# Performance work log

Measured on AMD Instinct MI355X. Metric: run time of the kernel, lower is better.

The kernel has to match this reference:

```python
import jax, jax.numpy as jnp
import numpy as np

ITERS = 10  # resonator iterations (iterations=10 in init_kwargs)

def _bipolar(key, shape):
    return jnp.where(jax.random.normal(key, shape) >= 0, 1.0, -1.0).astype(jnp.float32)

def setup_inputs() -> dict:
    key = jax.random.key(0)
    k1, k2, k3 = jax.random.split(key, 3)
    b, f, v, d = 64, 4, 256, 16384
    input_ = _bipolar(k1, (b, d))
    init_estimates = _bipolar(k2, (b, f, d))
    codebooks = _bipolar(k3, (f, v, d))
    return {"input": input_, "init_estimates": init_estimates, "codebooks": codebooks}

def _sign(x):
    # multiset quantize: bipolar sign (ties -> +1), matching MAP-VSA quantization
    return jnp.where(x >= 0, 1.0, -1.0).astype(x.dtype)

def reference(input, init_estimates, codebooks):
    """CONCURRENT resonator, SOFTWARE mode, activation=NONE, stoch=NONE.
    input: (b, d) bipolar; init_estimates: (b, f, d); codebooks: (f, v, d).
    For bipolar vectors: bind = elementwise *, inverse = identity, so
    multibind of all-but-factor-j equals (product over all f) * estimate_j
    (since e*e = 1). This replaces the roll+stack+multibind with one fused pass.
    """
    def step(est, _):
        total = jnp.prod(est, axis=-2, keepdims=True)        # (b, 1, d)
        inv_others = total * est                             # (b, f, d) product of other factors
        new_est = input[:, None, :] * inv_others             # unbind: (b, f, d)
        sim = jnp.einsum('bfd,fvd->bfv', new_est, codebooks) # dot_similarity
        # multiset(codebook, similarity, quantize=True): sign of similarity-weighted sum
        est_new = _sign(jnp.einsum('bfv,fvd->bfd', sim, codebooks))
        return est_new, None
    est, _ = jax.lax.scan(step, init_estimates, None, length=ITERS)
    # cleanup: argmax of |similarity| per factor (argmax_abs=True)
    sim = jnp.einsum('bfd,fvd->bfv', est, codebooks)
    outcome = jnp.argmax(jnp.abs(sim), axis=-1)              # (b, f) codeword indices
    return est, outcome
```

## Files before the change

### kernel.cpp

```cpp
#include <hip/hip_runtime.h>
#include <stdint.h>

typedef unsigned long long ull;
typedef unsigned short ushort_t;
typedef __attribute__((ext_vector_type(8))) short bf16x8;
typedef __attribute__((ext_vector_type(4))) float f32x4;


__global__ void pack_bits(const float* __restrict__ src, ull* __restrict__ dst, int nwords) {
    int gw   = (int)((blockIdx.x * blockDim.x + threadIdx.x) >> 6);
    int lane = threadIdx.x & 63;
    if (gw >= nwords) return;
    float x = src[(size_t)gw * 64 + lane];
    ull m = __ballot(x < 0.0f);
    if (lane == 0) dst[gw] = m;
}

__global__ void pack_cbw(const float* __restrict__ cb, ull* __restrict__ cbw) {
    int gw   = (int)((blockIdx.x * blockDim.x + threadIdx.x) >> 6);
    int lane = threadIdx.x & 63;
    int f = gw >> 16, rem = gw & 65535, w = rem >> 8, v = rem & 255;
    float x = cb[(size_t)(f * 256 + v) * 16384 + (size_t)w * 64 + lane];
    ull m = __ballot(x < 0.0f);
    if (lane == 0) cbw[(size_t)(f * 256 + w) * 256 + v] = m;
}

__global__ void pack_cbT(const ull* __restrict__ cbw, ull* __restrict__ cbT) {
    int gw   = (int)((blockIdx.x * blockDim.x + threadIdx.x) >> 6);
    int lane = threadIdx.x & 63;
    int f = gw >> 16, rem = gw & 65535, j = rem >> 14, d = rem & 16383;
    ull w = cbw[(size_t)(f * 256 + (d >> 6)) * 256 + j * 64 + lane];
    ull m = __ballot((w >> (d & 63)) & 1ull);
    if (lane == 0) cbT[(size_t)(f * 4 + j) * 16384 + d] = m;
}

__global__ void make_offc(const ull* __restrict__ cbT, int* __restrict__ offc) {
    int i = blockIdx.x * 256 + threadIdx.x;
    int f = i >> 14, d = i & 16383;
    int npop = 0;
    #pragma unroll
    for (int j = 0; j < 4; ++j) npop += __popcll(cbT[((size_t)f * 4 + j) * 16384 + d]);
    offc[i] = 8192 * (256 - 2 * npop);
}

__device__ __forceinline__ ushort_t f2bf(int x) {
    return (ushort_t)(__float_as_uint((float)x) >> 16);
}

__global__ __launch_bounds__(512) void simA_kernel(
        const ull* __restrict__ in_bits, const ull* __restrict__ est_in,
        const ull* __restrict__ cbw, ushort_t* __restrict__ simAB) {
    int b = blockIdx.x >> 2, f = blockIdx.x & 3;
    __shared__ ull s_ne[256];
    __shared__ short s_hp[2][256];
    int t = threadIdx.x;
    if (t < 256) {
        ull e0 = est_in[(size_t)(b * 4 + 0) * 256 + t];
        ull e1 = est_in[(size_t)(b * 4 + 1) * 256 + t];
        ull e2 = est_in[(size_t)(b * 4 + 2) * 256 + t];
        ull e3 = est_in[(size_t)(b * 4 + 3) * 256 + t];
        ull u  = in_bits[(size_t)b * 256 + t] ^ e0 ^ e1 ^ e2 ^ e3;
        ull ef = (f == 0) ? e0 : ((f == 1) ? e1 : ((f == 2) ? e2 : e3));
        s_ne[t] = u ^ ef;
    }
    __syncthreads();
    int v = t & 255, half = t >> 8;
    const ull* cw = cbw + (size_t)f * 65536 + (size_t)(half * 128) * 256 + v;
    int acc = 0;
    #pragma unroll 8
    for (int w = 0; w < 128; ++w)
        acc += __popcll(s_ne[half * 128 + w] ^ cw[(size_t)w * 256]);
    s_hp[half][v] = (short)acc;
    __syncthreads();
    if (t < 256) {
        int q = 16384 - (s_hp[0][t] + s_hp[1][t]);
        size_t base = ((size_t)(f * 64 + b)) * 512 + t;
        simAB[base]       = f2bf(q >> 8);
        simAB[base + 256] = f2bf(q & 255);
    }
}

__global__ __launch_bounds__(256) void gemm_kernel(
        const ull* __restrict__ cbT, const ushort_t* __restrict__ simAB,
        const int* __restrict__ offc, ull* __restrict__ est_out) {
    int f = blockIdx.x >> 6, dblk = blockIdx.x & 63;
    __shared__ int4 sB[8192];
    __shared__ unsigned char s_sign[64][256];
    __shared__ int s_off[256];
    int t = threadIdx.x;
    int lane = t & 63, wave = t >> 6;

    if (t < 256) s_off[t] = offc[f * 16384 + dblk * 256 + t];

    #pragma unroll 4
    for (int it = 0; it < 32; ++it) {
        int flat = it * 256 + t;
        int kc = flat >> 10, nt = (flat >> 6) & 15, l = flat & 63;
        int v0 = kc * 32 + ((l >> 4) << 3);
        int d  = dblk * 256 + nt * 16 + (l & 15);
        ull w = cbT[((size_t)f * 4 + (v0 >> 6)) * 16384 + d];
        unsigned bits = (unsigned)(w >> (v0 & 63)) & 0xFFu;
        int4 val;
        val.x = 0x3F803F80 | ((bits & 1u) << 15)        | ((bits & 2u) << 30);
        val.y = 0x3F803F80 | (((bits >> 2) & 1u) << 15) | (((bits >> 2) & 2u) << 30);
        val.z = 0x3F803F80 | (((bits >> 4) & 1u) << 15) | (((bits >> 4) & 2u) << 30);
        val.w = 0x3F803F80 | (((bits >> 6) & 1u) << 15) | (((bits >> 6) & 2u) << 30);
        sB[flat] = val;
    }

    bf16x8 Ahi[8], Alo[8];
    int m0 = wave * 16;
    const ushort_t* abase = simAB + ((size_t)(f * 64 + m0 + (lane & 15))) * 512 + ((lane >> 4) << 3);
    #pragma unroll
    for (int kc = 0; kc < 8; ++kc) {
        Ahi[kc] = *(const bf16x8*)(abase + kc * 32);
        Alo[kc] = *(const bf16x8*)(abase + 256 + kc * 32);
    }
    __syncthreads();

    for (int nt = 0; nt < 16; ++nt) {
        f32x4 acch = {0.f, 0.f, 0.f, 0.f}, accl = {0.f, 0.f, 0.f, 0.f};
        #pragma unroll
        for (int kc = 0; kc < 8; ++kc) {
            bf16x8 B = *(const bf16x8*)&sB[(kc * 16 + nt) * 64 + lane];
            acch = __builtin_amdgcn_mfma_f32_16x16x32_bf16(Ahi[kc], B, acch, 0, 0, 0);
            accl = __builtin_amdgcn_mfma_f32_16x16x32_bf16(Alo[kc], B, accl, 0, 0, 0);
        }
        int dl = nt * 16 + (lane & 15);
        float offf = (float)s_off[dl];
        #pragma unroll
        for (int r = 0; r < 4; ++r) {
            float S = 256.0f * acch[r] + accl[r];
            s_sign[m0 + ((lane >> 4) << 2) + r][dl] = (S < offf) ? 1 : 0;
        }
    }
    __syncthreads();

    if (t < 256) {
        int b = t >> 2, w = t & 3;
        ull m = 0;
        #pragma unroll
        for (int j2 = 0; j2 < 64; ++j2)
            m |= ((ull)s_sign[b][w * 64 + j2]) << j2;
        est_out[((size_t)(b * 4 + f)) * 256 + dblk * 4 + w] = m;
    }
}

__global__ __launch_bounds__(1024) void final_kernel(
        const ull* __restrict__ est, const ull* __restrict__ cbw, float* __restrict__ out) {
    int b = blockIdx.x >> 2, f = blockIdx.x & 3;
    __shared__ ull s_e[256];
    __shared__ int s_part[4][256];
    __shared__ int s_sim[256];
    int t = threadIdx.x;
    if (t < 256) s_e[t] = est[(size_t)(b * 4 + f) * 256 + t];
    __syncthreads();
    {
        int q = t >> 8, v = t & 255;
        const ull* cw = cbw + (size_t)f * 65536 + (size_t)(q * 64) * 256 + v;
        int acc = 0;
        #pragma unroll 8
        for (int w = 0; w < 64; ++w)
            acc += __popcll(s_e[q * 64 + w] ^ cw[(size_t)w * 256]);
        s_part[q][v] = acc;
    }
    __syncthreads();
    if (t < 256) {
        int h = s_part[0][t] + s_part[1][t] + s_part[2][t] + s_part[3][t];
        s_sim[t] = 16384 - 2 * h;
    }
    __syncthreads();
    int wv = t >> 6, lane = t & 63;
    if (wv == 0) {
        int best_a = -1, best_v = 0;
        #pragma unroll
        for (int c = 0; c < 4; ++c) {
            int v = c * 64 + lane;
            int sv = s_sim[v];
            int a = sv < 0 ? -sv : sv;
            if (a > best_a) { best_a = a; best_v = v; }
        }
        #pragma unroll
        for (int off = 1; off < 64; off <<= 1) {
            int oa = __shfl_xor(best_a, off);
            int ov = __shfl_xor(best_v, off);
            if (oa > best_a || (oa == best_a && ov < best_v)) { best_a = oa; best_v = ov; }
        }
        if (lane == 0) out[4194304 + b * 4 + f] = (float)best_v;
    }
    #pragma unroll
    for (int i = 0; i < 16; ++i) {
        int d = i * 1024 + t;
        ull w = s_e[d >> 6];
        out[((size_t)(b * 4 + f) << 14) + d] = ((w >> (d & 63)) & 1ull) ? -1.0f : 1.0f;
    }
}

extern "C" void kernel_launch(void* const* d_in, const int* in_sizes, int n_in,
                              void* d_out, int out_size, void* d_ws, size_t ws_size,
                              hipStream_t stream) {
    const float* input    = (const float*)d_in[0];
    const float* init_est = (const float*)d_in[1];
    const float* cb       = (const float*)d_in[2];
    float* out = (float*)d_out;
    char* ws = (char*)d_ws;

    ull* in_bits    = (ull*)(ws + 0);
    ull* est0       = (ull*)(ws + 131072);
    ull* est1       = (ull*)(ws + 655360);
    ull* cbw        = (ull*)(ws + 1179648);
    ull* cbT        = (ull*)(ws + 3276800);
    ushort_t* simAB = (ushort_t*)(ws + 5373952);
    int* offc       = (int*)(ws + 5636096);

    pack_bits<<<4096, 256, 0, stream>>>(input, in_bits, 16384);
    pack_bits<<<16384, 256, 0, stream>>>(init_est, est0, 65536);
    pack_cbw<<<65536, 256, 0, stream>>>(cb, cbw);
    pack_cbT<<<65536, 256, 0, stream>>>(cbw, cbT);
    make_offc<<<256, 256, 0, stream>>>(cbT, offc);

    ull* bufs[2] = { est0, est1 };
    for (int i = 0; i < 10; ++i) {
        simA_kernel<<<256, 512, 0, stream>>>(in_bits, bufs[i & 1], cbw, simAB);
        gemm_kernel<<<256, 256, 0, stream>>>(cbT, simAB, offc, bufs[(i & 1) ^ 1]);
    }
    final_kernel<<<256, 1024, 0, stream>>>(est0, cbw, out);
}
```

Before: 375.2 us.

## Merge pack kernels, widen blocks, ballot-pack gemm signs, fold offset into gemm

Merges the two input-packing launches into one and makes pack_cbw iterate in the read order of the float codebook so loads coalesce. The separate make_offc kernel is removed and its offsets are computed inside each gemm block. simA and gemm now run 1024 and 512 threads per block, with each gemm wave handling half the N tiles. Sign bits are packed with wave ballots instead of a byte array plus a serial OR loop. The intent is fewer launches, better coalescing and more parallelism per block, at the cost of offset work repeated in every iteration and more complex bit reassembly.

```diff
diff --git a/kernel.cpp b/kernel.cpp
--- a/kernel.cpp
+++ b/kernel.cpp
@@ -7,26 +7,34 @@
 typedef __attribute__((ext_vector_type(4))) float f32x4;
 
 
-__global__ void pack_bits(const float* __restrict__ src, ull* __restrict__ dst, int nwords) {
-    int gw   = (int)((blockIdx.x * blockDim.x + threadIdx.x) >> 6);
+__global__ __launch_bounds__(1024) void pack_all(
+        const float* __restrict__ in, const float* __restrict__ est_f,
+        ull* __restrict__ in_bits, ull* __restrict__ est_bits) {
+    int gw   = (int)((blockIdx.x * 1024 + threadIdx.x) >> 6);
     int lane = threadIdx.x & 63;
-    if (gw >= nwords) return;
-    float x = src[(size_t)gw * 64 + lane];
+    if (gw < 16384) {
+        float x = in[(size_t)gw * 64 + lane];
+        ull m = __ballot(x < 0.0f);
+        if (lane == 0) in_bits[gw] = m;
+    } else {
+        int g = gw - 16384;
+        float x = est_f[(size_t)g * 64 + lane];
+        ull m = __ballot(x < 0.0f);
+        if (lane == 0) est_bits[g] = m;
+    }
+}
+
+__global__ __launch_bounds__(1024) void pack_cbw(const float* __restrict__ cb, ull* __restrict__ cbw) {
+    int gw   = (int)((blockIdx.x * 1024 + threadIdx.x) >> 6);
+    int lane = threadIdx.x & 63;
+    int w = gw & 255, fv = gw >> 8;
+    float x = cb[(size_t)fv * 16384 + (size_t)w * 64 + lane];
     ull m = __ballot(x < 0.0f);
-    if (lane == 0) dst[gw] = m;
-}
-
-__global__ void pack_cbw(const float* __restrict__ cb, ull* __restrict__ cbw) {
-    int gw   = (int)((blockIdx.x * blockDim.x + threadIdx.x) >> 6);
-    int lane = threadIdx.x & 63;
-    int f = gw >> 16, rem = gw & 65535, w = rem >> 8, v = rem & 255;
-    float x = cb[(size_t)(f * 256 + v) * 16384 + (size_t)w * 64 + lane];
-    ull m = __ballot(x < 0.0f);
-    if (lane == 0) cbw[(size_t)(f * 256 + w) * 256 + v] = m;
-}
-
-__global__ void pack_cbT(const ull* __restrict__ cbw, ull* __restrict__ cbT) {
-    int gw   = (int)((blockIdx.x * blockDim.x + threadIdx.x) >> 6);
+    if (lane == 0) cbw[(size_t)((fv >> 8) * 256 + w) * 256 + (fv & 255)] = m;
+}
+
+__global__ __launch_bounds__(1024) void pack_cbT(const ull* __restrict__ cbw, ull* __restrict__ cbT) {
+    int gw   = (int)((blockIdx.x * 1024 + threadIdx.x) >> 6);
     int lane = threadIdx.x & 63;
     int f = gw >> 16, rem = gw & 65535, j = rem >> 14, d = rem & 16383;
     ull w = cbw[(size_t)(f * 256 + (d >> 6)) * 256 + j * 64 + lane];
@@ -34,71 +42,69 @@
     if (lane == 0) cbT[(size_t)(f * 4 + j) * 16384 + d] = m;
 }
 
-__global__ void make_offc(const ull* __restrict__ cbT, int* __restrict__ offc) {
-    int i = blockIdx.x * 256 + threadIdx.x;
-    int f = i >> 14, d = i & 16383;
-    int npop = 0;
-    #pragma unroll
-    for (int j = 0; j < 4; ++j) npop += __popcll(cbT[((size_t)f * 4 + j) * 16384 + d]);
-    offc[i] = 8192 * (256 - 2 * npop);
-}
-
 __device__ __forceinline__ ushort_t f2bf(int x) {
     return (ushort_t)(__float_as_uint((float)x) >> 16);
 }
 
-__global__ __launch_bounds__(512) void simA_kernel(
+__global__ __launch_bounds__(1024) void simA_kernel(
         const ull* __restrict__ in_bits, const ull* __restrict__ est_in,
         const ull* __restrict__ cbw, ushort_t* __restrict__ simAB) {
-    int b = blockIdx.x >> 2, f = blockIdx.x & 3;
+    int bA = blockIdx.x >> 2, fA = blockIdx.x & 3;
     __shared__ ull s_ne[256];
-    __shared__ short s_hp[2][256];
+    __shared__ short s_hp[4][256];
     int t = threadIdx.x;
     if (t < 256) {
-        ull e0 = est_in[(size_t)(b * 4 + 0) * 256 + t];
-        ull e1 = est_in[(size_t)(b * 4 + 1) * 256 + t];
-        ull e2 = est_in[(size_t)(b * 4 + 2) * 256 + t];
-        ull e3 = est_in[(size_t)(b * 4 + 3) * 256 + t];
-        ull u  = in_bits[(size_t)b * 256 + t] ^ e0 ^ e1 ^ e2 ^ e3;
-        ull ef = (f == 0) ? e0 : ((f == 1) ? e1 : ((f == 2) ? e2 : e3));
+        ull e0 = est_in[(size_t)(bA * 4 + 0) * 256 + t];
+        ull e1 = est_in[(size_t)(bA * 4 + 1) * 256 + t];
+        ull e2 = est_in[(size_t)(bA * 4 + 2) * 256 + t];
+        ull e3 = est_in[(size_t)(bA * 4 + 3) * 256 + t];
+        ull u  = in_bits[(size_t)bA * 256 + t] ^ e0 ^ e1 ^ e2 ^ e3;
+        ull ef = (fA == 0) ? e0 : ((fA == 1) ? e1 : ((fA == 2) ? e2 : e3));
         s_ne[t] = u ^ ef;
     }
     __syncthreads();
-    int v = t & 255, half = t >> 8;
-    const ull* cw = cbw + (size_t)f * 65536 + (size_t)(half * 128) * 256 + v;
-    int acc = 0;
-    #pragma unroll 8
-    for (int w = 0; w < 128; ++w)
-        acc += __popcll(s_ne[half * 128 + w] ^ cw[(size_t)w * 256]);
-    s_hp[half][v] = (short)acc;
-    __syncthreads();
-    if (t < 256) {
-        int q = 16384 - (s_hp[0][t] + s_hp[1][t]);
-        size_t base = ((size_t)(f * 64 + b)) * 512 + t;
+    {
+        int v = t & 255, qr = t >> 8;
+        const ull* cw = cbw + (size_t)fA * 65536 + (size_t)(qr * 64) * 256 + v;
+        int acc = 0;
+        #pragma unroll 16
+        for (int w = 0; w < 64; ++w)
+            acc += __popcll(s_ne[qr * 64 + w] ^ cw[(size_t)w * 256]);
+        s_hp[qr][v] = (short)acc;
+    }
+    __syncthreads();
+    if (t < 256) {
+        int q = 16384 - (s_hp[0][t] + s_hp[1][t] + s_hp[2][t] + s_hp[3][t]);
+        size_t base = ((size_t)(fA * 64 + bA)) * 512 + t;
         simAB[base]       = f2bf(q >> 8);
         simAB[base + 256] = f2bf(q & 255);
     }
 }
 
-__global__ __launch_bounds__(256) void gemm_kernel(
+__global__ __launch_bounds__(512) void gemm_kernel(
         const ull* __restrict__ cbT, const ushort_t* __restrict__ simAB,
-        const int* __restrict__ offc, ull* __restrict__ est_out) {
-    int f = blockIdx.x >> 6, dblk = blockIdx.x & 63;
+        ull* __restrict__ est_out) {
+    int fB = blockIdx.x >> 6, dblk = blockIdx.x & 63;
     __shared__ int4 sB[8192];
-    __shared__ unsigned char s_sign[64][256];
+    __shared__ ull s_ball[8][8][4];
     __shared__ int s_off[256];
-    int t = threadIdx.x;
-    int lane = t & 63, wave = t >> 6;
-
-    if (t < 256) s_off[t] = offc[f * 16384 + dblk * 256 + t];
+    int t = threadIdx.x, lane = t & 63, wave = t >> 6;
+
+    if (t < 256) {
+        int d = dblk * 256 + t;
+        int npop = 0;
+        #pragma unroll
+        for (int j = 0; j < 4; ++j) npop += __popcll(cbT[((size_t)fB * 4 + j) * 16384 + d]);
+        s_off[t] = 8192 * (256 - 2 * npop);
+    }
 
     #pragma unroll 4
-    for (int it = 0; it < 32; ++it) {
-        int flat = it * 256 + t;
+    for (int it = 0; it < 16; ++it) {
+        int flat = it * 512 + t;
         int kc = flat >> 10, nt = (flat >> 6) & 15, l = flat & 63;
         int v0 = kc * 32 + ((l >> 4) << 3);
         int d  = dblk * 256 + nt * 16 + (l & 15);
-        ull w = cbT[((size_t)f * 4 + (v0 >> 6)) * 16384 + d];
+        ull w = cbT[((size_t)fB * 4 + (v0 >> 6)) * 16384 + d];
         unsigned bits = (unsigned)(w >> (v0 & 63)) & 0xFFu;
         int4 val;
         val.x = 0x3F803F80 | ((bits & 1u) << 15)        | ((bits & 2u) << 30);
@@ -108,9 +114,10 @@
         sB[flat] = val;
     }
 
+    int mw = wave & 3, ntb = (wave >> 2) << 3;
+    const ushort_t* abase = simAB
+        + ((size_t)(fB * 64 + mw * 16 + (lane & 15))) * 512 + ((lane >> 4) << 3);
     bf16x8 Ahi[8], Alo[8];
-    int m0 = wave * 16;
-    const ushort_t* abase = simAB + ((size_t)(f * 64 + m0 + (lane & 15))) * 512 + ((lane >> 4) << 3);
     #pragma unroll
     for (int kc = 0; kc < 8; ++kc) {
         Ahi[kc] = *(const bf16x8*)(abase + kc * 32);
@@ -118,7 +125,9 @@
     }
     __syncthreads();
 
-    for (int nt = 0; nt < 16; ++nt) {
+    #pragma unroll 2
+    for (int ntl = 0; ntl < 8; ++ntl) {
+        int nt = ntb + ntl;
         f32x4 acch = {0.f, 0.f, 0.f, 0.f}, accl = {0.f, 0.f, 0.f, 0.f};
         #pragma unroll
         for (int kc = 0; kc < 8; ++kc) {
@@ -126,23 +135,27 @@
             acch = __builtin_amdgcn_mfma_f32_16x16x32_bf16(Ahi[kc], B, acch, 0, 0, 0);
             accl = __builtin_amdgcn_mfma_f32_16x16x32_bf16(Alo[kc], B, accl, 0, 0, 0);
         }
-        int dl = nt * 16 + (lane & 15);
-        float offf = (float)s_off[dl];
+        float offf = (float)s_off[nt * 16 + (lane & 15)];
         #pragma unroll
         for (int r = 0; r < 4; ++r) {
             float S = 256.0f * acch[r] + accl[r];
-            s_sign[m0 + ((lane >> 4) << 2) + r][dl] = (S < offf) ? 1 : 0;
-        }
-    }
-    __syncthreads();
-
-    if (t < 256) {
-        int b = t >> 2, w = t & 3;
-        ull m = 0;
-        #pragma unroll
-        for (int j2 = 0; j2 < 64; ++j2)
-            m |= ((ull)s_sign[b][w * 64 + j2]) << j2;
-        est_out[((size_t)(b * 4 + f)) * 256 + dblk * 4 + w] = m;
+            ull m = __ballot(S < offf);
+            if (lane == 0) s_ball[wave][nt & 7][r] = m;
+        }
+    }
+    __syncthreads();
+
+    if (t < 256) {
+        int b = t >> 2, w4 = t & 3;
+        int wv = (b >> 4) + ((w4 >= 2) ? 4 : 0);
+        ull word = 0;
+        #pragma unroll
+        for (int k = 0; k < 4; ++k) {
+            int nt = w4 * 4 + k;
+            ull m = s_ball[wv][nt & 7][b & 3];
+            word |= ((m >> (((b >> 2) & 3) * 16)) & 0xFFFFull) << (k * 16);
+        }
+        est_out[((size_t)(b * 4 + fB)) * 256 + dblk * 4 + w4] = word;
     }
 }
 
@@ -150,23 +163,23 @@
         const ull* __restrict__ est, const ull* __restrict__ cbw, float* __restrict__ out) {
     int b = blockIdx.x >> 2, f = blockIdx.x & 3;
     __shared__ ull s_e[256];
-    __shared__ int s_part[4][256];
+    __shared__ short s_hp[4][256];
     __shared__ int s_sim[256];
     int t = threadIdx.x;
     if (t < 256) s_e[t] = est[(size_t)(b * 4 + f) * 256 + t];
     __syncthreads();
     {
-        int q = t >> 8, v = t & 255;
-        const ull* cw = cbw + (size_t)f * 65536 + (size_t)(q * 64) * 256 + v;
+        int v = t & 255, qr = t >> 8;
+        const ull* cw = cbw + (size_t)f * 65536 + (size_t)(qr * 64) * 256 + v;
         int acc = 0;
-        #pragma unroll 8
+        #pragma unroll 16
         for (int w = 0; w < 64; ++w)
-            acc += __popcll(s_e[q * 64 + w] ^ cw[(size_t)w * 256]);
-        s_part[q][v] = acc;
-    }
-    __syncthreads();
-    if (t < 256) {
-        int h = s_part[0][t] + s_part[1][t] + s_part[2][t] + s_part[3][t];
+            acc += __popcll(s_e[qr * 64 + w] ^ cw[(size_t)w * 256]);
+        s_hp[qr][v] = (short)acc;
+    }
+    __syncthreads();
+    if (t < 256) {
+        int h = s_hp[0][t] + s_hp[1][t] + s_hp[2][t] + s_hp[3][t];
         s_sim[t] = 16384 - 2 * h;
     }
     __syncthreads();
@@ -211,18 +224,15 @@
     ull* cbw        = (ull*)(ws + 1179648);
     ull* cbT        = (ull*)(ws + 3276800);
     ushort_t* simAB = (ushort_t*)(ws + 5373952);
-    int* offc       = (int*)(ws + 5636096);
-
-    pack_bits<<<4096, 256, 0, stream>>>(input, in_bits, 16384);
-    pack_bits<<<16384, 256, 0, stream>>>(init_est, est0, 65536);
-    pack_cbw<<<65536, 256, 0, stream>>>(cb, cbw);
-    pack_cbT<<<65536, 256, 0, stream>>>(cbw, cbT);
-    make_offc<<<256, 256, 0, stream>>>(cbT, offc);
+
+    pack_all<<<5120, 1024, 0, stream>>>(input, init_est, in_bits, est0);
+    pack_cbw<<<16384, 1024, 0, stream>>>(cb, cbw);
+    pack_cbT<<<16384, 1024, 0, stream>>>(cbw, cbT);
 
     ull* bufs[2] = { est0, est1 };
     for (int i = 0; i < 10; ++i) {
-        simA_kernel<<<256, 512, 0, stream>>>(in_bits, bufs[i & 1], cbw, simAB);
-        gemm_kernel<<<256, 256, 0, stream>>>(cbT, simAB, offc, bufs[(i & 1) ^ 1]);
+        simA_kernel<<<256, 1024, 0, stream>>>(in_bits, bufs[i & 1], cbw, simAB);
+        gemm_kernel<<<256, 512, 0, stream>>>(cbT, simAB, bufs[(i & 1) ^ 1]);
     }
     final_kernel<<<256, 1024, 0, stream>>>(est0, cbw, out);
 }
```

Result: no change. 378.2 us (+0.8%).
